# Kernel optimization log

Hardware: AMD Instinct MI355X
Metric: run time of the kernel (lower is better)

Reference implementation:

```python
import jax, jax.numpy as jnp
from jax import lax
import numpy as np

SCALE_N = 4
KERN = 5
PAD = KERN // 2
_G = np.float32([[0.003765, 0.015019, 0.023792, 0.015019, 0.003765],
                 [0.015019, 0.059912, 0.094907, 0.059912, 0.015019],
                 [0.023792, 0.094907, 0.150342, 0.094907, 0.023792],
                 [0.015019, 0.059912, 0.094907, 0.059912, 0.015019],
                 [0.003765, 0.015019, 0.023792, 0.015019, 0.003765]])
FILTER = jnp.asarray(_G)


def _lap_split(img):
    N, c, H, W = img.shape
    f = jnp.broadcast_to(FILTER, (c, 1, KERN, KERN))
    smooth = lax.conv_general_dilated(img, f, (1, 1), [(PAD, PAD), (PAD, PAD)],
                                      feature_group_count=c)
    lo = smooth[:, :, ::2, ::2]
    oph, opw = (H + 1) % 2, (W + 1) % 2
    # conv_transpose2d(stride=2, padding=PAD, output_padding) as lhs-dilated conv
    # (Gaussian kernel is symmetric, so no spatial flip needed)
    lo2 = 4.0 * lax.conv_general_dilated(
        lo, f, (1, 1),
        [(KERN - 1 - PAD, KERN - 1 - PAD + oph), (KERN - 1 - PAD, KERN - 1 - PAD + opw)],
        lhs_dilation=(2, 2), feature_group_count=c)
    hi = img - lo2
    return lo, hi


def _pyramid(img):
    levels = []
    for _ in range(SCALE_N):
        img, hi = _lap_split(img)
        levels.append(hi)
    levels.append(img)
    return levels


def _sample_points(img, xs, ys):
    # bilinear grid_sample, align_corners=False, zero padding.
    # img: (N,C,H,W); xs, ys: (P,) normalized coords in [-1,1]. -> (N,C,P)
    N, C, H, W = img.shape
    fx = ((xs + 1.0) * W - 1.0) * 0.5
    fy = ((ys + 1.0) * H - 1.0) * 0.5
    x0 = jnp.floor(fx)
    y0 = jnp.floor(fy)
    wx = fx - x0
    wy = fy - y0
    x0i = x0.astype(jnp.int32)
    y0i = y0.astype(jnp.int32)
    out = jnp.zeros((N, C, xs.shape[0]), img.dtype)
    corners = [(0, 0, (1 - wx) * (1 - wy)), (1, 0, wx * (1 - wy)),
               (0, 1, (1 - wx) * wy), (1, 1, wx * wy)]
    for dx, dy, w in corners:
        xc = x0i + dx
        yc = y0i + dy
        valid = (xc >= 0) & (xc < W) & (yc >= 0) & (yc < H)
        xcc = jnp.clip(xc, 0, W - 1)
        ycc = jnp.clip(yc, 0, H - 1)
        vals = img[:, :, ycc, xcc]  # (N,C,P) gather
        out = out + vals * (w * valid)[None, None, :]
    return out


def setup_inputs() -> dict:
    key = jax.random.key(0)
    k1, k2, k3 = jax.random.split(key, 3)
    N, c, H, W = 64, 32, 128, 128
    outdims = 4096
    m = SCALE_N + 1
    x = jax.random.normal(k1, (N, c, H, W), dtype=jnp.float32)
    grid = jax.random.uniform(k2, (1, outdims, 1, 2), minval=-0.1, maxval=0.1,
                              dtype=jnp.float32)
    features = (jnp.full((1, m * c, 1, outdims), 1.0 / c, jnp.float32)
                + 0.01 * jax.random.normal(k3, (1, m * c, 1, outdims), jnp.float32))
    bias = jnp.zeros((outdims,), jnp.float32)
    return {"x": x, "grid": grid, "features": features, "bias": bias}


def reference(x, grid, features, bias):
    N, c, H, W = x.shape
    m = SCALE_N + 1
    outdims = grid.shape[1]
    g = jnp.clip(grid, -1.0, 1.0)
    xs = g[0, :, 0, 0]  # width coord
    ys = g[0, :, 0, 1]  # height coord
    levels = _pyramid(x)
    pools = [_sample_points(lv, xs, ys) for lv in levels]  # each (N,c,P)
    y = jnp.concatenate(pools, axis=1)  # (N, m*c, P)
    feat = features.reshape(1, m * c, outdims)
    y = (y * feat).sum(axis=1)  # (N, P)
    return y + bias
```

## Files before the change

### kernel.cpp

```cpp
#include <hip/hip_runtime.h>
#include <hip/hip_fp16.h>


#define P1 66
#define P2 34
#define P3 18
#define P4 10
#define OFF_LO1 0
#define OFF_LO2 4224
#define OFF_LO3 5312
#define OFF_LO4 5600
#define SLOT    5680

#define G_A 0.0613609f
#define G_B 0.2447700f
#define G_C 0.3877386f

#define T_FOFF 16384

static __device__ __forceinline__ float clampf(float v, float lo, float hi) {
    return fminf(fmaxf(v, lo), hi);
}
static __device__ __forceinline__ int imin(int a, int b) { return a < b ? a : b; }
static __device__ __forceinline__ int imax(int a, int b) { return a > b ? a : b; }

static __device__ __forceinline__ unsigned int pack_h2(float a, float b) {
    __half ha = __float2half_rn(a), hb = __float2half_rn(b);
    unsigned short ua = *(unsigned short*)&ha, ub = *(unsigned short*)&hb;
    return (unsigned int)ua | ((unsigned int)ub << 16);
}
static __device__ __forceinline__ unsigned int pack_u2(int a, int b) {
    return (unsigned int)(a & 0xffff) | ((unsigned int)b << 16);
}
static __device__ __forceinline__ float2 uph2(unsigned int u) {
    unsigned short lo = (unsigned short)(u & 0xffff), hi = (unsigned short)(u >> 16);
    __half hl = *(__half*)&lo, hh = *(__half*)&hi;
    return make_float2(__half2float(hl), __half2float(hh));
}

__global__ void init_out_kernel(const float* __restrict__ bias, float* __restrict__ y) {
    int i = blockIdx.x * blockDim.x + threadIdx.x;
    y[i] = bias[i & 4095];
}

__global__ void weights_kernel(const float* __restrict__ grid, float* __restrict__ ws) {
    int out = blockIdx.x * blockDim.x + threadIdx.x;
    if (out >= 4096) return;
    float xs = clampf(grid[2 * out + 0], -1.f, 1.f);
    float ys = clampf(grid[2 * out + 1], -1.f, 1.f);

    uint4* L0 = (uint4*)ws;
    uint2* T  = (uint2*)(ws + T_FOFF);

    float fx = (xs + 1.f) * 64.f - 0.5f;
    float fy = (ys + 1.f) * 64.f - 0.5f;
    float x0f = floorf(fx), y0f = floorf(fy);
    int x0 = (int)x0f, y0 = (int)y0f;
    float wx = fx - x0f, wy = fy - y0f;
    float ux0 = (x0 >= 0)      ? (1.f - wx) : 0.f;
    float ux1 = (x0 + 1 < 128) ? wx         : 0.f;
    float uy0 = (y0 >= 0)      ? (1.f - wy) : 0.f;
    float uy1 = (y0 + 1 < 128) ? wy         : 0.f;
    int cx0 = imax(x0, 0), cx1 = imin(x0 + 1, 127);
    int cy0 = imax(y0, 0), cy1 = imin(y0 + 1, 127);
    L0[out] = make_uint4(pack_h2(ux0 * uy0, ux1 * uy0),
                         pack_h2(ux0 * uy1, ux1 * uy1),
                         pack_u2(cy0 * 128 + cx0, cy0 * 128 + cx1),
                         pack_u2(cy1 * 128 + cx0, cy1 * 128 + cx1));

    int   x0p = x0, y0p = y0;
    float ux0p = ux0, ux1p = ux1, uy0p = uy0, uy1p = uy1;

    const int offs[4]    = {OFF_LO1, OFF_LO2, OFF_LO3, OFF_LO4};
    const int strides[4] = {P1, P2, P3, P4};

    for (int j = 1; j <= 4; ++j) {
        const int Wj = 128 >> j, Pj = strides[j - 1], off = offs[j - 1];

        int qx; float a0, a1, a2;
        if (x0p & 1) { qx = (x0p - 1) >> 1;
            a0 = G_B * ux0p + G_A * ux1p; a1 = G_B * ux0p + G_C * ux1p; a2 = G_A * ux1p; }
        else         { qx = (x0p >> 1) - 1;
            a0 = G_A * ux0p; a1 = G_C * ux0p + G_B * ux1p; a2 = G_A * ux0p + G_B * ux1p; }
        int qy; float e0, e1, e2;
        if (y0p & 1) { qy = (y0p - 1) >> 1;
            e0 = G_B * uy0p + G_A * uy1p; e1 = G_B * uy0p + G_C * uy1p; e2 = G_A * uy1p; }
        else         { qy = (y0p >> 1) - 1;
            e0 = G_A * uy0p; e1 = G_C * uy0p + G_B * uy1p; e2 = G_A * uy0p + G_B * uy1p; }

        float half = (float)(Wj >> 1);
        float fxj = (xs + 1.f) * half - 0.5f;
        float fyj = (ys + 1.f) * half - 0.5f;
        float x0jf = floorf(fxj), y0jf = floorf(fyj);
        int x0j = (int)x0jf, y0j = (int)y0jf;
        float wxj = fxj - x0jf, wyj = fyj - y0jf;
        float ux0j = (x0j >= 0)     ? (1.f - wxj) : 0.f;
        float ux1j = (x0j + 1 < Wj) ? wxj         : 0.f;
        float uy0j = (y0j >= 0)     ? (1.f - wyj) : 0.f;
        float uy1j = (y0j + 1 < Wj) ? wyj         : 0.f;

        int bxb = qx & ~1;
        bxb = imin(imax(bxb, 0), Wj - 4);

        float axv[4], bxv[4], ayv[3], byv[3];
        int rv[3];
#pragma unroll
        for (int t = 0; t < 4; ++t) {
            int col = bxb + t;
            int s = col - qx;
            float av = (s == 0) ? a0 : (s == 1) ? a1 : (s == 2) ? a2 : 0.f;
            if (s < 0 || s > 2) av = 0.f;
            int sb = col - x0j;
            float bv = (sb == 0) ? ux0j : (sb == 1) ? ux1j : 0.f;
            axv[t] = av;
            bxv[t] = bv;
        }
#pragma unroll
        for (int t = 0; t < 3; ++t) {
            int row = qy + t;
            bool v = (row >= 0) && (row < Wj);
            float av = (t == 0) ? e0 : (t == 1) ? e1 : e2;
            ayv[t] = v ? av : 0.f;
            int sb = row - y0j;
            byv[t] = (sb == 0) ? uy0j : (sb == 1) ? uy1j : 0.f;
            int rc = imin(imax(row, 0), Wj - 1);
            rv[t] = off + rc * Pj + bxb;
        }

        int tb = (j - 1) * 5 * 4096 + out;
        T[tb]            = make_uint2(pack_h2(axv[0], axv[1]), pack_h2(axv[2], axv[3]));
        T[tb + 4096]     = make_uint2(pack_h2(bxv[0], bxv[1]), pack_h2(bxv[2], bxv[3]));
        T[tb + 2 * 4096] = make_uint2(pack_h2(ayv[0], ayv[1]), pack_h2(ayv[2], 0.f));
        T[tb + 3 * 4096] = make_uint2(pack_h2(byv[0], byv[1]), pack_h2(byv[2], 0.f));
        T[tb + 4 * 4096] = make_uint2(pack_u2(rv[0], rv[1]), pack_u2(rv[2], 0));

        x0p = x0j; y0p = y0j;
        ux0p = ux0j; ux1p = ux1j; uy0p = uy0j; uy1p = uy1j;
    }
}

static __device__ __forceinline__ float down_pt_lds(const float* s, int stride, int S,
                                                    int i, int j) {
    const float g1[5] = {G_A, G_B, G_C, G_B, G_A};
    int by = 2 * i - 2, bx = 2 * j - 2;
    float acc = 0.f;
    if (by >= 0 && by + 4 < S && bx >= 0 && bx + 4 < S) {
#pragma unroll
        for (int dy = 0; dy < 5; ++dy) {
            const float* r = s + (by + dy) * stride + bx;
            acc += g1[dy] * (G_A * (r[0] + r[4]) + G_B * (r[1] + r[3]) + G_C * r[2]);
        }
    } else {
#pragma unroll
        for (int dy = 0; dy < 5; ++dy) {
            int yy = by + dy;
            if ((unsigned)yy < (unsigned)S) {
#pragma unroll
                for (int dx = 0; dx < 5; ++dx) {
                    int xx = bx + dx;
                    if ((unsigned)xx < (unsigned)S)
                        acc += g1[dy] * g1[dx] * s[yy * stride + xx];
                }
            }
        }
    }
    return acc;
}

__global__ __launch_bounds__(256, 6) void pyr_sample_kernel(
    const float* __restrict__ x, const float* __restrict__ wrec,
    const float* __restrict__ feat, float* __restrict__ y)
{
    __shared__ __align__(16) float s_lo[SLOT];
    const int tid = threadIdx.x;
    const int n   = blockIdx.x >> 5;
    const int c   = blockIdx.x & 31;
    const float* img = x + ((size_t)(n * 32 + c) << 14);

    const float g1[5] = {G_A, G_B, G_C, G_B, G_A};

    for (int r = tid; r < 1024; r += 256) {
        int i = r >> 4, j0 = (r & 15) << 2;
        int by = 2 * i - 2;
        float acc[4] = {0.f, 0.f, 0.f, 0.f};
        if (i >= 1 && i <= 62 && j0 >= 4 && j0 <= 56) {
            const int a = 2 * j0 - 4;
#pragma unroll
            for (int dy = 0; dy < 5; ++dy) {
                const float* rp = img + (by + dy) * 128 + a;
                float4 q0 = *(const float4*)(rp);
                float4 q1 = *(const float4*)(rp + 4);
                float4 q2 = *(const float4*)(rp + 8);
                float4 q3 = *(const float4*)(rp + 12);
                float s2 = q0.z, s3 = q0.w, s4 = q1.x, s5 = q1.y, s6 = q1.z,
                      s7 = q1.w, s8 = q2.x, s9 = q2.y, s10 = q2.z, s11 = q2.w,
                      s12 = q3.x;
                float g = g1[dy];
                acc[0] += g * (G_A * (s2 + s6)  + G_B * (s3 + s5)  + G_C * s4);
                acc[1] += g * (G_A * (s4 + s8)  + G_B * (s5 + s7)  + G_C * s6);
                acc[2] += g * (G_A * (s6 + s10) + G_B * (s7 + s9)  + G_C * s8);
                acc[3] += g * (G_A * (s8 + s12) + G_B * (s9 + s11) + G_C * s10);
            }
        } else {
            int bx = 2 * j0 - 2;
#pragma unroll
            for (int dy = 0; dy < 5; ++dy) {
                int yy = by + dy;
                if ((unsigned)yy < 128u) {
#pragma unroll
                    for (int t = 0; t < 11; ++t) {
                        int xx = bx + t;
                        if ((unsigned)xx < 128u) {
                            float v = img[yy * 128 + xx];
#pragma unroll
                            for (int jj = 0; jj < 4; ++jj) {
                                int dx = t - 2 * jj;
                                if (dx >= 0 && dx <= 4) acc[jj] += g1[dy] * g1[dx] * v;
                            }
                        }
                    }
                }
            }
        }
        int base = OFF_LO1 + i * P1 + j0;
        *(float2*)&s_lo[base]     = make_float2(acc[0], acc[1]);
        *(float2*)&s_lo[base + 2] = make_float2(acc[2], acc[3]);
    }
    __syncthreads();

    for (int p = tid; p < 1024; p += 256) {
        int i = p >> 5, j = p & 31;
        s_lo[OFF_LO2 + i * P2 + j] = down_pt_lds(s_lo + OFF_LO1, P1, 64, i, j);
    }
    __syncthreads();

    {
        int i = tid >> 4, j = tid & 15;
        s_lo[OFF_LO3 + i * P3 + j] = down_pt_lds(s_lo + OFF_LO2, P2, 32, i, j);
    }
    __syncthreads();

    if (tid < 64) {
        int i = tid >> 3, j = tid & 7;
        s_lo[OFF_LO4 + i * P4 + j] = down_pt_lds(s_lo + OFF_LO3, P3, 16, i, j);
    }
    __syncthreads();

    const uint4* L0 = (const uint4*)wrec;
    const uint2* T  = (const uint2*)(wrec + T_FOFF);
    float* yrow = y + ((size_t)n << 12);
    for (int out = tid; out < 4096; out += 256) {
        uint4 h0 = L0[out];
        float2 wA = uph2(h0.x), wB = uph2(h0.y);
        int o00 = (int)(h0.z & 0xffff), o01 = (int)(h0.z >> 16);
        int o10 = (int)(h0.w & 0xffff), o11 = (int)(h0.w >> 16);

        float f_prev = feat[((size_t)c << 12) + out];
        float v0 = wA.x * img[o00] + wA.y * img[o01] + wB.x * img[o10] + wB.y * img[o11];
        float acc = f_prev * v0;

#pragma unroll
        for (int j = 1; j <= 4; ++j) {
            const int tb = (j - 1) * 5 * 4096 + out;
            uint2 uAX = T[tb];
            uint2 uBX = T[tb + 4096];
            uint2 uAY = T[tb + 2 * 4096];
            uint2 uBY = T[tb + 3 * 4096];
            uint2 uR  = T[tb + 4 * 4096];
            float2 ax01 = uph2(uAX.x), ax23 = uph2(uAX.y);
            float2 bx01 = uph2(uBX.x), bx23 = uph2(uBX.y);
            float2 ay01 = uph2(uAY.x); float ay2 = uph2(uAY.y).x;
            float2 by01 = uph2(uBY.x); float by2 = uph2(uBY.y).x;
            int r0 = (int)(uR.x & 0xffff), r1 = (int)(uR.x >> 16), r2 = (int)(uR.y & 0xffff);

            float f_cur = feat[((size_t)(j * 32 + c) << 12) + out];

            float2 p0a = *(const float2*)&s_lo[r0];
            float2 p0b = *(const float2*)&s_lo[r0 + 2];
            float2 p1a = *(const float2*)&s_lo[r1];
            float2 p1b = *(const float2*)&s_lo[r1 + 2];
            float2 p2a = *(const float2*)&s_lo[r2];
            float2 p2b = *(const float2*)&s_lo[r2 + 2];
            float ra0 = ax01.x * p0a.x + ax01.y * p0a.y + ax23.x * p0b.x + ax23.y * p0b.y;
            float ra1 = ax01.x * p1a.x + ax01.y * p1a.y + ax23.x * p1b.x + ax23.y * p1b.y;
            float ra2 = ax01.x * p2a.x + ax01.y * p2a.y + ax23.x * p2b.x + ax23.y * p2b.y;
            float rb0 = bx01.x * p0a.x + bx01.y * p0a.y + bx23.x * p0b.x + bx23.y * p0b.y;
            float rb1 = bx01.x * p1a.x + bx01.y * p1a.y + bx23.x * p1b.x + bx23.y * p1b.y;
            float rb2 = bx01.x * p2a.x + bx01.y * p2a.y + bx23.x * p2b.x + bx23.y * p2b.y;
            float sa = ay01.x * ra0 + ay01.y * ra1 + ay2 * ra2;
            float sb = by01.x * rb0 + by01.y * rb1 + by2 * rb2;
            acc += f_cur * sb - 4.f * f_prev * sa;
            f_prev = f_cur;
        }
        atomicAdd(&yrow[out], acc);
    }
}

extern "C" void kernel_launch(void* const* d_in, const int* in_sizes, int n_in,
                              void* d_out, int out_size, void* d_ws, size_t ws_size,
                              hipStream_t stream) {
    (void)in_sizes; (void)n_in; (void)ws_size;
    const float* x    = (const float*)d_in[0];
    const float* grid = (const float*)d_in[1];
    const float* feat = (const float*)d_in[2];
    const float* bias = (const float*)d_in[3];
    float* y  = (float*)d_out;
    float* ws = (float*)d_ws;

    weights_kernel<<<16, 256, 0, stream>>>(grid, ws);
    init_out_kernel<<<out_size / 256, 256, 0, stream>>>(bias, y);
    pyr_sample_kernel<<<2048, 256, 0, stream>>>(x, ws, feat, y);
}
```

Baseline: 404.9 us.

## Split pyramid build and gather into two kernels to drop output atomics

Builds each image's low-pass pyramid in one kernel and stores it to workspace. A second kernel assigns one output tile per block, loops over all 32 channels with double-buffered LDS loading of the stored pyramids, keeps the per-output weights in registers, and writes y directly with bias instead of using atomicAdd. This removes the atomic contention and the repeated weight-table reloads per channel. The cost is extra global traffic of about 46MB for the pyramid round trip and an extra launch. The old fused path stays as a fallback when the workspace is too small.

```diff
diff --git a/kernel.cpp b/kernel.cpp
--- a/kernel.cpp
+++ b/kernel.cpp
@@ -11,12 +11,15 @@
 #define OFF_LO3 5312
 #define OFF_LO4 5600
 #define SLOT    5680
+#define SLOT4   1420
 
 #define G_A 0.0613609f
 #define G_B 0.2447700f
 #define G_C 0.3877386f
 
-#define T_FOFF 16384
+#define T_FOFF   16384
+#define PYR_FOFF 196608
+#define PSTRIDE  5696
 
 static __device__ __forceinline__ float clampf(float v, float lo, float hi) {
     return fminf(fmaxf(v, lo), hi);
@@ -167,16 +170,8 @@
     return acc;
 }
 
-__global__ __launch_bounds__(256, 6) void pyr_sample_kernel(
-    const float* __restrict__ x, const float* __restrict__ wrec,
-    const float* __restrict__ feat, float* __restrict__ y)
-{
-    __shared__ __align__(16) float s_lo[SLOT];
-    const int tid = threadIdx.x;
-    const int n   = blockIdx.x >> 5;
-    const int c   = blockIdx.x & 31;
-    const float* img = x + ((size_t)(n * 32 + c) << 14);
-
+static __device__ __forceinline__ void build_pyramid(const float* __restrict__ img,
+                                                     float* __restrict__ s_lo, int tid) {
     const float g1[5] = {G_A, G_B, G_C, G_B, G_A};
 
     for (int r = tid; r < 1024; r += 256) {
@@ -245,6 +240,150 @@
         s_lo[OFF_LO4 + i * P4 + j] = down_pt_lds(s_lo + OFF_LO3, P3, 16, i, j);
     }
     __syncthreads();
+}
+
+__global__ __launch_bounds__(256) void pyr_build_kernel(
+    const float* __restrict__ x, float* __restrict__ ws)
+{
+    __shared__ __align__(16) float s_lo[SLOT];
+    const int tid = threadIdx.x;
+    const int bid = blockIdx.x;
+    const float* img = x + ((size_t)bid << 14);
+
+    build_pyramid(img, s_lo, tid);
+
+    float4* g4 = (float4*)(ws + PYR_FOFF + (size_t)bid * PSTRIDE);
+    const float4* s4 = (const float4*)s_lo;
+    for (int i = tid; i < SLOT4; i += 256) g4[i] = s4[i];
+}
+
+__global__ __launch_bounds__(256) void pyr_gather_kernel(
+    const float* __restrict__ x, const float* __restrict__ wrec,
+    const float* __restrict__ feat, const float* __restrict__ bias,
+    float* __restrict__ y)
+{
+    __shared__ __align__(16) float s_p[2][PSTRIDE];
+    const int tid  = threadIdx.x;
+    const int n    = blockIdx.x >> 4;
+    const int tile = blockIdx.x & 15;
+    const int out  = (tile << 8) + tid;
+
+    const uint4* L0 = (const uint4*)wrec;
+    const uint2* T  = (const uint2*)(wrec + T_FOFF);
+
+    uint4 h0 = L0[out];
+    float2 wA = uph2(h0.x), wB = uph2(h0.y);
+    int o00 = (int)(h0.z & 0xffff), o01 = (int)(h0.z >> 16);
+    int o10 = (int)(h0.w & 0xffff), o11 = (int)(h0.w >> 16);
+
+    float ax[4][4], bx[4][4], ay[4][3], by[4][3];
+    int   rv[4][3];
+#pragma unroll
+    for (int j = 0; j < 4; ++j) {
+        const int tb = j * 5 * 4096 + out;
+        uint2 uAX = T[tb];
+        uint2 uBX = T[tb + 4096];
+        uint2 uAY = T[tb + 2 * 4096];
+        uint2 uBY = T[tb + 3 * 4096];
+        uint2 uR  = T[tb + 4 * 4096];
+        float2 t;
+        t = uph2(uAX.x); ax[j][0] = t.x; ax[j][1] = t.y;
+        t = uph2(uAX.y); ax[j][2] = t.x; ax[j][3] = t.y;
+        t = uph2(uBX.x); bx[j][0] = t.x; bx[j][1] = t.y;
+        t = uph2(uBX.y); bx[j][2] = t.x; bx[j][3] = t.y;
+        t = uph2(uAY.x); ay[j][0] = t.x; ay[j][1] = t.y;
+        ay[j][2] = uph2(uAY.y).x;
+        t = uph2(uBY.x); by[j][0] = t.x; by[j][1] = t.y;
+        by[j][2] = uph2(uBY.y).x;
+        rv[j][0] = (int)(uR.x & 0xffff);
+        rv[j][1] = (int)(uR.x >> 16);
+        rv[j][2] = (int)(uR.y & 0xffff);
+    }
+
+    const float* img_n = x + ((size_t)n << 19);
+    const float* pyr_n = wrec + PYR_FOFF + (size_t)n * 32 * PSTRIDE;
+
+    {
+        const float4* g = (const float4*)pyr_n;
+        float4* d = (float4*)s_p[0];
+        for (int i = tid; i < SLOT4; i += 256) d[i] = g[i];
+    }
+    __syncthreads();
+
+    float acc = 0.f;
+#pragma unroll 1
+    for (int c = 0; c < 32; ++c) {
+        const int cur = c & 1;
+
+        float4 st0, st1, st2, st3, st4, st5;
+        const bool have_next = (c + 1 < 32);
+        if (have_next) {
+            const float4* g = (const float4*)(pyr_n + (size_t)(c + 1) * PSTRIDE);
+            int i0 = tid;
+            st0 = g[i0];
+            st1 = g[i0 + 256];
+            st2 = g[i0 + 512];
+            st3 = g[i0 + 768];
+            st4 = g[i0 + 1024];
+            st5 = (i0 + 1280 < SLOT4) ? g[i0 + 1280] : make_float4(0.f, 0.f, 0.f, 0.f);
+        }
+
+        const float* sl  = s_p[cur];
+        const float* img = img_n + ((size_t)c << 14);
+        float f_prev = feat[((size_t)c << 12) + out];
+        float v0 = wA.x * img[o00] + wA.y * img[o01] + wB.x * img[o10] + wB.y * img[o11];
+        float a = f_prev * v0;
+
+#pragma unroll
+        for (int j = 0; j < 4; ++j) {
+            float f_cur = feat[((size_t)((j + 1) * 32 + c) << 12) + out];
+            int r0 = rv[j][0], r1 = rv[j][1], r2 = rv[j][2];
+            float2 p0a = *(const float2*)(sl + r0);
+            float2 p0b = *(const float2*)(sl + r0 + 2);
+            float2 p1a = *(const float2*)(sl + r1);
+            float2 p1b = *(const float2*)(sl + r1 + 2);
+            float2 p2a = *(const float2*)(sl + r2);
+            float2 p2b = *(const float2*)(sl + r2 + 2);
+            float ra0 = ax[j][0] * p0a.x + ax[j][1] * p0a.y + ax[j][2] * p0b.x + ax[j][3] * p0b.y;
+            float ra1 = ax[j][0] * p1a.x + ax[j][1] * p1a.y + ax[j][2] * p1b.x + ax[j][3] * p1b.y;
+            float ra2 = ax[j][0] * p2a.x + ax[j][1] * p2a.y + ax[j][2] * p2b.x + ax[j][3] * p2b.y;
+            float rb0 = bx[j][0] * p0a.x + bx[j][1] * p0a.y + bx[j][2] * p0b.x + bx[j][3] * p0b.y;
+            float rb1 = bx[j][0] * p1a.x + bx[j][1] * p1a.y + bx[j][2] * p1b.x + bx[j][3] * p1b.y;
+            float rb2 = bx[j][0] * p2a.x + bx[j][1] * p2a.y + bx[j][2] * p2b.x + bx[j][3] * p2b.y;
+            float sa = ay[j][0] * ra0 + ay[j][1] * ra1 + ay[j][2] * ra2;
+            float sb = by[j][0] * rb0 + by[j][1] * rb1 + by[j][2] * rb2;
+            a += f_cur * sb - 4.f * f_prev * sa;
+            f_prev = f_cur;
+        }
+        acc += a;
+
+        if (have_next) {
+            float4* d = (float4*)s_p[cur ^ 1];
+            int i0 = tid;
+            d[i0]        = st0;
+            d[i0 + 256]  = st1;
+            d[i0 + 512]  = st2;
+            d[i0 + 768]  = st3;
+            d[i0 + 1024] = st4;
+            if (i0 + 1280 < SLOT4) d[i0 + 1280] = st5;
+        }
+        __syncthreads();
+    }
+
+    y[((size_t)n << 12) + out] = acc + bias[out];
+}
+
+__global__ __launch_bounds__(256, 3) void pyr_sample_fused(
+    const float* __restrict__ x, const float* __restrict__ wrec,
+    const float* __restrict__ feat, float* __restrict__ y)
+{
+    __shared__ __align__(16) float s_lo[SLOT];
+    const int tid = threadIdx.x;
+    const int n   = blockIdx.x >> 5;
+    const int c   = blockIdx.x & 31;
+    const float* img = x + ((size_t)(n * 32 + c) << 14);
+
+    build_pyramid(img, s_lo, tid);
 
     const uint4* L0 = (const uint4*)wrec;
     const uint2* T  = (const uint2*)(wrec + T_FOFF);
@@ -299,7 +438,7 @@
 extern "C" void kernel_launch(void* const* d_in, const int* in_sizes, int n_in,
                               void* d_out, int out_size, void* d_ws, size_t ws_size,
                               hipStream_t stream) {
-    (void)in_sizes; (void)n_in; (void)ws_size;
+    (void)in_sizes; (void)n_in;
     const float* x    = (const float*)d_in[0];
     const float* grid = (const float*)d_in[1];
     const float* feat = (const float*)d_in[2];
@@ -307,7 +446,14 @@
     float* y  = (float*)d_out;
     float* ws = (float*)d_ws;
 
+    const size_t NEED = sizeof(float) * ((size_t)PYR_FOFF + 2048ull * PSTRIDE);
+
     weights_kernel<<<16, 256, 0, stream>>>(grid, ws);
-    init_out_kernel<<<out_size / 256, 256, 0, stream>>>(bias, y);
-    pyr_sample_kernel<<<2048, 256, 0, stream>>>(x, ws, feat, y);
-}
+    if (ws_size >= NEED) {
+        pyr_build_kernel<<<2048, 256, 0, stream>>>(x, ws);
+        pyr_gather_kernel<<<1024, 256, 0, stream>>>(x, ws, feat, bias, y);
+    } else {
+        init_out_kernel<<<out_size / 256, 256, 0, stream>>>(bias, y);
+        pyr_sample_fused<<<2048, 256, 0, stream>>>(x, ws, feat, y);
+    }
+}
```

New measurement: 365.3 us. 9.8% less time.
